# Kernel tuning notes

Measured on AMD Instinct MI355X. Metric: run time of the kernel, lower is better.

Reference implementation:

```python
import jax, jax.numpy as jnp
import numpy as np

COMMITMENT_COST = 0.25


def setup_inputs() -> dict:
    key = jax.random.key(0)
    k1, k2 = jax.random.split(key)
    N, K, D = 131072, 1024, 64
    inputs = jax.random.normal(k1, (N, D), dtype=jnp.float32)
    # torch init: uniform(-1/K, 1/K); use randn scaled similarly-small for a generic table
    embedding = jax.random.uniform(k2, (K, D), dtype=jnp.float32,
                                   minval=-1.0 / K, maxval=1.0 / K)
    return {"inputs": inputs, "embedding": embedding}


def reference(inputs, embedding):
    distances = (jnp.sum(inputs ** 2, axis=1, keepdims=True)
                 + jnp.sum(embedding ** 2, axis=1)
                 - 2.0 * inputs @ embedding.T)
    encoding_indices = jnp.argmin(distances, axis=1)            # [N]
    # direct gather (same math as one-hot @ embedding)
    quantized = embedding[encoding_indices]                     # [N, D]

    diff2 = jnp.mean((quantized - inputs) ** 2)
    # e_latent_loss == q_latent_loss numerically in fwd
    loss = diff2 + COMMITMENT_COST * diff2

    # straight-through output (forward value == quantized)
    quantized_st = inputs + jax.lax.stop_gradient(quantized - inputs)

    # avg_probs via histogram instead of materializing [N, K] one-hot
    N, K = inputs.shape[0], embedding.shape[0]
    counts = jnp.zeros((K,), dtype=jnp.float32).at[encoding_indices].add(1.0)
    avg_probs = counts / N
    perplexity = jnp.exp(-jnp.sum(avg_probs * jnp.log(avg_probs + 1e-10)))

    return quantized_st, loss, encoding_indices.reshape(N, 1), perplexity
```

## Files before the change

kernel.cpp:

```cpp
#include <hip/hip_runtime.h>
#include <hip/hip_bf16.h>

#define D 64
#define MARGIN 4e-5f
#define KS 2

typedef __attribute__((ext_vector_type(8))) short bf16x8;
typedef __attribute__((ext_vector_type(4))) float f32x4;
typedef __attribute__((ext_vector_type(4))) unsigned uint4v;


__device__ __forceinline__ float np_pairwise_sumsq64(const float* a) {
    float r[8];
#pragma unroll
    for (int j = 0; j < 8; ++j) r[j] = __fmul_rn(a[j], a[j]);
#pragma unroll
    for (int i = 8; i < 64; i += 8)
#pragma unroll
        for (int j = 0; j < 8; ++j)
            r[j] = __fadd_rn(r[j], __fmul_rn(a[i + j], a[i + j]));
    return __fadd_rn(
        __fadd_rn(__fadd_rn(r[0], r[1]), __fadd_rn(r[2], r[3])),
        __fadd_rn(__fadd_rn(r[4], r[5]), __fadd_rn(r[6], r[7])));
}

#define CVT8(F0, F1, H, L)                                                    \
    do {                                                                      \
        float _f[8] = {F0.x, F0.y, F0.z, F0.w, F1.x, F1.y, F1.z, F1.w};       \
        _Pragma("unroll") for (int _i = 0; _i < 8; ++_i) {                    \
            unsigned _u = __float_as_uint(_f[_i]);                            \
            unsigned _hb = (_u + 0x7fffu + ((_u >> 16) & 1u)) >> 16;          \
            float _hf = __uint_as_float(_hb << 16);                           \
            float _r = _f[_i] - _hf;                                          \
            unsigned _u2 = __float_as_uint(_r);                               \
            unsigned _lb = (_u2 + 0x7fffu + ((_u2 >> 16) & 1u)) >> 16;        \
            H[_i] = (short)_hb;                                               \
            L[_i] = (short)_lb;                                               \
        }                                                                     \
    } while (0)

__global__ __launch_bounds__(256) void vq_prep_all(
    const float* __restrict__ emb, int K,
    float* __restrict__ eenp, float* __restrict__ neh,
    unsigned short* __restrict__ ehs, float* __restrict__ eT) {
    int b = blockIdx.x;
    if (b < 64) {
        int t = b * 256 + threadIdx.x;
        int tile = t >> 8, r = t & 255, s = r >> 6, l = r & 63;
        int sub = l & 15, grp = l >> 4;
        int k = tile * 16 + sub;
        int d0 = ((s & 1) << 5) + (grp << 3);
        const float* e = emb + (size_t)k * D + d0;
        float4 f0 = *(const float4*)e;
        float4 f1 = *(const float4*)(e + 4);
        bf16x8 h, lo;
        CVT8(f0, f1, h, lo);
        *(bf16x8*)(ehs + (size_t)t * 8) = (s >> 1) ? lo : h;
    } else if (b < 68) {
        int k = (b - 64) * 256 + threadIdx.x;
        float s = np_pairwise_sumsq64(emb + (size_t)k * D);
        eenp[k] = s;
        neh[k] = -0.5f * s;
    } else {
        int t = (b - 68) * 256 + threadIdx.x;
        int d = t / K, k = t - d * K;
        eT[t] = emb[(size_t)k * D + d];
    }
}

__global__ __launch_bounds__(256) void vq_screen(
    const float* __restrict__ x, const unsigned short* __restrict__ ehs,
    const float* __restrict__ neh, int N, int K,
    float* __restrict__ m1p, float* __restrict__ m2p, int* __restrict__ bip,
    float* __restrict__ xxp) {
    const int tid = threadIdx.x;
    const int lane = tid & 63;
    const int wid = tid >> 6;
    const int kslice = blockIdx.x & (KS - 1);
    const int rowblk = blockIdx.x >> 1;
    const int row0 = rowblk * 256 + wid * 64;
    const int sub = lane & 15, grp = lane >> 4;
    const int g4 = grp << 2;
    const int k0 = kslice * (K / KS);
    const int NT = (K / KS) >> 4;
    const int t0 = k0 >> 4;

    __shared__ __align__(16) unsigned short lds[2][2048];

    bf16x8 xh[4][2], xl[4][2];
    float xq[4];
#pragma unroll
    for (int rt = 0; rt < 4; ++rt) {
        xq[rt] = 0.f;
        const float* xrow = x + (((size_t)(row0 + (rt << 4) + sub)) << 6) + (grp << 3);
#pragma unroll
        for (int s = 0; s < 2; ++s) {
            float4 f0 = *(const float4*)(xrow + (s << 5));
            float4 f1 = *(const float4*)(xrow + (s << 5) + 4);
            xq[rt] = fmaf(f0.x, f0.x, xq[rt]); xq[rt] = fmaf(f0.y, f0.y, xq[rt]);
            xq[rt] = fmaf(f0.z, f0.z, xq[rt]); xq[rt] = fmaf(f0.w, f0.w, xq[rt]);
            xq[rt] = fmaf(f1.x, f1.x, xq[rt]); xq[rt] = fmaf(f1.y, f1.y, xq[rt]);
            xq[rt] = fmaf(f1.z, f1.z, xq[rt]); xq[rt] = fmaf(f1.w, f1.w, xq[rt]);
            CVT8(f0, f1, xh[rt][s], xl[rt][s]);
        }
    }
#pragma unroll
    for (int rt = 0; rt < 4; ++rt) {
        xq[rt] += __shfl_xor(xq[rt], 16);
        xq[rt] += __shfl_xor(xq[rt], 32);
    }

    float m1[4], m2[4];
    int bi[4];
#pragma unroll
    for (int rt = 0; rt < 4; ++rt) { m1[rt] = -3e38f; m2[rt] = -3e38f; bi[rt] = 0; }

    const unsigned short* sbase = ehs + ((size_t)t0 << 11);
    const int slot = (wid << 9) + (lane << 3);

    uint4v tmp = *(const uint4v*)(sbase + slot);
    *(uint4v*)&lds[0][slot] = tmp;
    __syncthreads();

    for (int t = 0; t < NT; ++t) {
        const int cur = t & 1;
        if (t + 1 < NT)
            tmp = *(const uint4v*)(sbase + ((size_t)(t + 1) << 11) + slot);

        f32x4 cb = *(const f32x4*)(neh + k0 + (t << 4) + g4);
        const bf16x8* L = (const bf16x8*)&lds[cur][0];
        bf16x8 a0 = L[lane];
        bf16x8 a1 = L[64 + lane];
        bf16x8 a2 = L[128 + lane];
        bf16x8 a3 = L[192 + lane];

        f32x4 acc[4];
#pragma unroll
        for (int rt = 0; rt < 4; ++rt)
            acc[rt] = __builtin_amdgcn_mfma_f32_16x16x32_bf16(a0, xh[rt][0], cb, 0, 0, 0);
#pragma unroll
        for (int rt = 0; rt < 4; ++rt)
            acc[rt] = __builtin_amdgcn_mfma_f32_16x16x32_bf16(a2, xh[rt][0], acc[rt], 0, 0, 0);
#pragma unroll
        for (int rt = 0; rt < 4; ++rt)
            acc[rt] = __builtin_amdgcn_mfma_f32_16x16x32_bf16(a0, xl[rt][0], acc[rt], 0, 0, 0);
#pragma unroll
        for (int rt = 0; rt < 4; ++rt)
            acc[rt] = __builtin_amdgcn_mfma_f32_16x16x32_bf16(a1, xh[rt][1], acc[rt], 0, 0, 0);
#pragma unroll
        for (int rt = 0; rt < 4; ++rt)
            acc[rt] = __builtin_amdgcn_mfma_f32_16x16x32_bf16(a3, xh[rt][1], acc[rt], 0, 0, 0);
#pragma unroll
        for (int rt = 0; rt < 4; ++rt)
            acc[rt] = __builtin_amdgcn_mfma_f32_16x16x32_bf16(a1, xl[rt][1], acc[rt], 0, 0, 0);

        int cbase = k0 + (t << 4) + g4;
#pragma unroll
        for (int rt = 0; rt < 4; ++rt) {
#pragma unroll
            for (int j = 0; j < 4; ++j) {
                float v = acc[rt][j];
                int c = cbase + j;
                bool tk = v > m1[rt];
                m2[rt] = fminf(fmaxf(v, m2[rt]), m1[rt]);
                m1[rt] = tk ? v : m1[rt];
                bi[rt] = tk ? c : bi[rt];
            }
        }

        if (t + 1 < NT)
            *(uint4v*)&lds[cur ^ 1][slot] = tmp;
        __syncthreads();
    }

#pragma unroll
    for (int rt = 0; rt < 4; ++rt) {
#pragma unroll
        for (int off = 16; off <= 32; off <<= 1) {
            float om1 = __shfl_xor(m1[rt], off);
            float om2 = __shfl_xor(m2[rt], off);
            int obi = __shfl_xor(bi[rt], off);
            bool take = (om1 > m1[rt]) || (om1 == m1[rt] && obi < bi[rt]);
            m2[rt] = fmaxf(fminf(om1, m1[rt]), fmaxf(om2, m2[rt]));
            m1[rt] = take ? om1 : m1[rt];
            bi[rt] = take ? obi : bi[rt];
        }
    }

    if (lane < 16) {
#pragma unroll
        for (int rt = 0; rt < 4; ++rt) {
            size_t idx = (size_t)kslice * N + row0 + (rt << 4) + lane;
            m1p[idx] = m1[rt];
            m2p[idx] = m2[rt];
            bip[idx] = bi[rt];
            if (kslice == 0) xxp[row0 + (rt << 4) + lane] = xq[rt];
        }
    }
}

__global__ __launch_bounds__(256) void vq_epilogue(
    const float* __restrict__ x, const float* __restrict__ emb,
    const float* __restrict__ eT, const float* __restrict__ eenp,
    const float* __restrict__ m1p, const float* __restrict__ m2p,
    const int* __restrict__ bip, const float* __restrict__ xxp, int N, int K,
    float* __restrict__ outq, float* __restrict__ outidx,
    double* __restrict__ loss) {
    const int tid = threadIdx.x;
    const int rows0 = blockIdx.x * 64;
    __shared__ int sdec[64];
    __shared__ int samb[64];
    __shared__ int snamb;
    __shared__ float sxrow[64];
    __shared__ float swm[4];
    __shared__ int swi[4];

    if (tid == 0) snamb = 0;

    if (tid < 64) {
        int r = rows0 + tid;
        float gm1 = m1p[r], gm2 = m2p[r];
        int gbi = bip[r];
        {
            size_t idx = (size_t)N + r;
            float m1b = m1p[idx], m2b = m2p[idx];
            int bb = bip[idx];
            bool take = m1b > gm1;
            gm2 = fmaxf(fminf(gm1, m1b), fmaxf(gm2, m2b));
            gm1 = take ? m1b : gm1;
            gbi = take ? bb : gbi;
        }
        int dec = gbi;
        double lpart = 0.0;
        if (2.0f * (gm1 - gm2) < MARGIN) {
            int pos = atomicAdd(&snamb, 1);
            samb[pos] = tid;
            dec = -1;
        } else {
            outidx[r] = (float)dec;
            lpart = (double)(xxp[r] - 2.0f * gm1);
        }
        sdec[tid] = dec;
#pragma unroll
        for (int off = 32; off; off >>= 1) lpart += __shfl_down(lpart, off);
        if (tid == 0) atomicAdd(loss, lpart);
    }
    __syncthreads();

    const int namb = snamb;
    const int w = tid >> 6, l = tid & 63;
    const int c4 = (w << 6) + l;
    const f32x4* eT4 = (const f32x4*)eT;
    for (int j = 0; j < namb; ++j) {
        int lr = samb[j];
        int row = rows0 + lr;
        if (tid < 64) sxrow[tid] = x[(size_t)row * D + tid];
        __syncthreads();
        float xx = np_pairwise_sumsq64(sxrow);
        f32x4 dt = (f32x4){0.f, 0.f, 0.f, 0.f};
#pragma unroll 8
        for (int d = 0; d < D; ++d) {
            f32x4 ev = eT4[(size_t)d * 256 + c4];
            float xv = sxrow[d];
            dt[0] = __fmaf_rn(xv, ev[0], dt[0]);
            dt[1] = __fmaf_rn(xv, ev[1], dt[1]);
            dt[2] = __fmaf_rn(xv, ev[2], dt[2]);
            dt[3] = __fmaf_rn(xv, ev[3], dt[3]);
        }
        float bm = 1e30f;
        int bi = 0;
#pragma unroll
        for (int jj = 0; jj < 4; ++jj) {
            int k = (c4 << 2) + jj;
            float dist = __fsub_rn(__fadd_rn(xx, eenp[k]),
                                   __fmul_rn(2.0f, dt[jj]));
            if (dist < bm) { bm = dist; bi = k; }
        }
#pragma unroll
        for (int off = 1; off < 64; off <<= 1) {
            float ov = __shfl_xor(bm, off);
            int oi = __shfl_xor(bi, off);
            if (ov < bm || (ov == bm && oi < bi)) { bm = ov; bi = oi; }
        }
        if (l == 0) { swm[w] = bm; swi[w] = bi; }
        __syncthreads();
        if (tid == 0) {
            float fm = swm[0];
            int fi = swi[0];
#pragma unroll
            for (int ww = 1; ww < 4; ++ww) {
                float ov = swm[ww];
                int oi = swi[ww];
                if (ov < fm || (ov == fm && oi < fi)) { fm = ov; fi = oi; }
            }
            sdec[lr] = fi;
            outidx[row] = (float)fi;
            atomicAdd(loss, (double)fm);
        }
        __syncthreads();
    }

    const int chunk = tid & 15, rl = tid >> 4;
#pragma unroll
    for (int p = 0; p < 4; ++p) {
        int lr = p * 16 + rl;
        int dp = sdec[lr];
        if (dp >= 0) {
            float4 ev = *(const float4*)(emb + (size_t)dp * D + chunk * 4);
            *(float4*)(outq + (size_t)(rows0 + lr) * D + chunk * 4) = ev;
        }
    }
}

__global__ __launch_bounds__(256) void vq_histperp(
    const float* __restrict__ outidx, int N, int K,
    unsigned* __restrict__ counts, unsigned* __restrict__ done,
    const double* __restrict__ loss,
    float* __restrict__ out_loss, float* __restrict__ out_perp) {
    __shared__ unsigned h[1024];
    __shared__ unsigned rank_s;
#pragma unroll
    for (int i = 0; i < 4; ++i) h[threadIdx.x + 256 * i] = 0;
    __syncthreads();
    int per = N / gridDim.x;
    int base = blockIdx.x * per;
    for (int i = threadIdx.x; i < per; i += 256) {
        int k = (int)outidx[base + i];
        atomicAdd(&h[k], 1u);
    }
    __syncthreads();
#pragma unroll
    for (int i = 0; i < 4; ++i) {
        int b = threadIdx.x + 256 * i;
        unsigned v = h[b];
        if (b < K && v) atomicAdd(counts + b, v);
    }
    __threadfence();
    if (threadIdx.x == 0) rank_s = atomicAdd(done, 1u);
    __syncthreads();
    if (rank_s == gridDim.x - 1) {
        double part = 0.0;
        for (int k = threadIdx.x; k < K; k += 256) {
            unsigned c = atomicAdd(counts + k, 0u);
            double p = (double)c / (double)N;
            part += p * log(p + 1e-10);
        }
#pragma unroll
        for (int off = 32; off; off >>= 1) part += __shfl_down(part, off);
        __shared__ double ls[4];
        if ((threadIdx.x & 63) == 0) ls[threadIdx.x >> 6] = part;
        __syncthreads();
        if (threadIdx.x == 0) {
            double s = ls[0] + ls[1] + ls[2] + ls[3];
            *out_perp = (float)exp(-s);
            double diff2 = *loss / ((double)N * (double)D);
            *out_loss = (float)(1.25 * diff2);
        }
    }
}

extern "C" void kernel_launch(void* const* d_in, const int* in_sizes, int n_in,
                              void* d_out, int out_size, void* d_ws, size_t ws_size,
                              hipStream_t stream) {
    const float* x = (const float*)d_in[0];
    const float* emb = (const float*)d_in[1];
    int N = in_sizes[0] / D;
    int K = in_sizes[1] / D;

    float* outq = (float*)d_out;
    float* out_loss = outq + (size_t)N * D;
    float* outidx = out_loss + 1;
    float* out_perp = outidx + N;

    char* ws = (char*)d_ws;
    unsigned* counts = (unsigned*)ws;
    unsigned* done = (unsigned*)(ws + (size_t)K * 4);
    double* loss = (double*)(ws + (size_t)K * 4 + 8);
    float* neh = (float*)(ws + (size_t)K * 4 + 16);
    float* eenp = (float*)(ws + (size_t)K * 8 + 16);
    unsigned short* ehs = (unsigned short*)(ws + (size_t)K * 12 + 16);
    float* eT = (float*)(ws + (size_t)K * 12 + 16 + (size_t)K * 256);
    size_t poff = (size_t)K * 12 + 16 + (size_t)K * 256 + (size_t)K * D * 4;
    float* m1p = (float*)(ws + poff);
    float* m2p = (float*)(ws + poff + (size_t)KS * N * 4);
    int* bip = (int*)(ws + poff + (size_t)KS * N * 8);
    float* xxp = (float*)(ws + poff + (size_t)KS * N * 12);

    hipMemsetAsync(d_ws, 0, (size_t)K * 4 + 16, stream);

    vq_prep_all<<<64 + 4 + (K * D + 255) / 256, 256, 0, stream>>>(
        emb, K, eenp, neh, ehs, eT);
    vq_screen<<<(N / 256) * KS, 256, 0, stream>>>(x, ehs, neh, N, K,
                                                  m1p, m2p, bip, xxp);
    vq_epilogue<<<N / 64, 256, 0, stream>>>(x, emb, eT, eenp, m1p, m2p, bip,
                                            xxp, N, K, outq, outidx, loss);
    vq_histperp<<<16, 256, 0, stream>>>(outidx, N, K, counts, done, loss,
                                        out_loss, out_perp);
}
```

Measured before the change: 177.9 us.

## Move ambiguous-row fp32 rescoring into separate compacted-worklist kernel

```diff
diff --git a/kernel.cpp b/kernel.cpp
--- a/kernel.cpp
+++ b/kernel.cpp
@@ -200,22 +200,15 @@
 }
 
 __global__ __launch_bounds__(256) void vq_epilogue(
-    const float* __restrict__ x, const float* __restrict__ emb,
-    const float* __restrict__ eT, const float* __restrict__ eenp,
+    const float* __restrict__ emb,
     const float* __restrict__ m1p, const float* __restrict__ m2p,
-    const int* __restrict__ bip, const float* __restrict__ xxp, int N, int K,
+    const int* __restrict__ bip, const float* __restrict__ xxp, int N,
     float* __restrict__ outq, float* __restrict__ outidx,
-    double* __restrict__ loss) {
+    double* __restrict__ lossA,
+    unsigned* __restrict__ nunc, unsigned* __restrict__ list) {
     const int tid = threadIdx.x;
     const int rows0 = blockIdx.x * 64;
     __shared__ int sdec[64];
-    __shared__ int samb[64];
-    __shared__ int snamb;
-    __shared__ float sxrow[64];
-    __shared__ float swm[4];
-    __shared__ int swi[4];
-
-    if (tid == 0) snamb = 0;
 
     if (tid < 64) {
         int r = rows0 + tid;
@@ -230,11 +223,17 @@
             gm1 = take ? m1b : gm1;
             gbi = take ? bb : gbi;
         }
+        bool amb = 2.0f * (gm1 - gm2) < MARGIN;
+        unsigned long long mask = __ballot(amb);
+        int cnt = __popcll(mask);
+        unsigned base = 0;
+        if (tid == 0 && cnt) base = atomicAdd(nunc, (unsigned)cnt);
+        base = __shfl(base, 0);
         int dec = gbi;
         double lpart = 0.0;
-        if (2.0f * (gm1 - gm2) < MARGIN) {
-            int pos = atomicAdd(&snamb, 1);
-            samb[pos] = tid;
+        if (amb) {
+            int rank = __popcll(mask & ((1ull << tid) - 1ull));
+            list[base + rank] = (unsigned)r;
             dec = -1;
         } else {
             outidx[r] = (float)dec;
@@ -243,62 +242,9 @@
         sdec[tid] = dec;
 #pragma unroll
         for (int off = 32; off; off >>= 1) lpart += __shfl_down(lpart, off);
-        if (tid == 0) atomicAdd(loss, lpart);
-    }
-    __syncthreads();
-
-    const int namb = snamb;
-    const int w = tid >> 6, l = tid & 63;
-    const int c4 = (w << 6) + l;
-    const f32x4* eT4 = (const f32x4*)eT;
-    for (int j = 0; j < namb; ++j) {
-        int lr = samb[j];
-        int row = rows0 + lr;
-        if (tid < 64) sxrow[tid] = x[(size_t)row * D + tid];
-        __syncthreads();
-        float xx = np_pairwise_sumsq64(sxrow);
-        f32x4 dt = (f32x4){0.f, 0.f, 0.f, 0.f};
-#pragma unroll 8
-        for (int d = 0; d < D; ++d) {
-            f32x4 ev = eT4[(size_t)d * 256 + c4];
-            float xv = sxrow[d];
-            dt[0] = __fmaf_rn(xv, ev[0], dt[0]);
-            dt[1] = __fmaf_rn(xv, ev[1], dt[1]);
-            dt[2] = __fmaf_rn(xv, ev[2], dt[2]);
-            dt[3] = __fmaf_rn(xv, ev[3], dt[3]);
-        }
-        float bm = 1e30f;
-        int bi = 0;
-#pragma unroll
-        for (int jj = 0; jj < 4; ++jj) {
-            int k = (c4 << 2) + jj;
-            float dist = __fsub_rn(__fadd_rn(xx, eenp[k]),
-                                   __fmul_rn(2.0f, dt[jj]));
-            if (dist < bm) { bm = dist; bi = k; }
-        }
-#pragma unroll
-        for (int off = 1; off < 64; off <<= 1) {
-            float ov = __shfl_xor(bm, off);
-            int oi = __shfl_xor(bi, off);
-            if (ov < bm || (ov == bm && oi < bi)) { bm = ov; bi = oi; }
-        }
-        if (l == 0) { swm[w] = bm; swi[w] = bi; }
-        __syncthreads();
-        if (tid == 0) {
-            float fm = swm[0];
-            int fi = swi[0];
-#pragma unroll
-            for (int ww = 1; ww < 4; ++ww) {
-                float ov = swm[ww];
-                int oi = swi[ww];
-                if (ov < fm || (ov == fm && oi < fi)) { fm = ov; fi = oi; }
-            }
-            sdec[lr] = fi;
-            outidx[row] = (float)fi;
-            atomicAdd(loss, (double)fm);
-        }
-        __syncthreads();
-    }
+        if (tid == 0) lossA[blockIdx.x] = lpart;
+    }
+    __syncthreads();
 
     const int chunk = tid & 15, rl = tid >> 4;
 #pragma unroll
@@ -312,10 +258,81 @@
     }
 }
 
+__global__ __launch_bounds__(256) void vq_resolve(
+    const float* __restrict__ x, const float* __restrict__ emb,
+    const float* __restrict__ eT, const float* __restrict__ eenp,
+    int N, int K,
+    float* __restrict__ outq, float* __restrict__ outidx,
+    double* __restrict__ lossR,
+    const unsigned* __restrict__ nunc, const unsigned* __restrict__ list) {
+    const unsigned n = *nunc;
+    const int w = threadIdx.x >> 6, lane = threadIdx.x & 63;
+    const f32x4* eT4 = (const f32x4*)eT;
+    double lp = 0.0;
+    for (unsigned i = blockIdx.x * 4 + w; i < n; i += gridDim.x * 4) {
+        const int r = (int)list[i];
+        float xr[D];
+        {
+            const float4* xp = (const float4*)(x + (size_t)r * D);
+#pragma unroll
+            for (int jj = 0; jj < D / 4; ++jj) {
+                float4 v = xp[jj];
+                xr[4 * jj + 0] = v.x; xr[4 * jj + 1] = v.y;
+                xr[4 * jj + 2] = v.z; xr[4 * jj + 3] = v.w;
+            }
+        }
+        float xx = np_pairwise_sumsq64(xr);
+        f32x4 dt[4];
+#pragma unroll
+        for (int kk = 0; kk < 4; ++kk) dt[kk] = (f32x4){0.f, 0.f, 0.f, 0.f};
+#pragma unroll 4
+        for (int d = 0; d < D; ++d) {
+            float xv = xr[d];
+#pragma unroll
+            for (int kk = 0; kk < 4; ++kk) {
+                f32x4 ev = eT4[(size_t)d * 256 + kk * 64 + lane];
+                dt[kk][0] = __fmaf_rn(xv, ev[0], dt[kk][0]);
+                dt[kk][1] = __fmaf_rn(xv, ev[1], dt[kk][1]);
+                dt[kk][2] = __fmaf_rn(xv, ev[2], dt[kk][2]);
+                dt[kk][3] = __fmaf_rn(xv, ev[3], dt[kk][3]);
+            }
+        }
+        float bm = 1e30f;
+        int bi = 0;
+#pragma unroll
+        for (int kk = 0; kk < 4; ++kk)
+#pragma unroll
+            for (int jj = 0; jj < 4; ++jj) {
+                int k = kk * 256 + lane * 4 + jj;
+                float dist = __fsub_rn(__fadd_rn(xx, eenp[k]),
+                                       __fmul_rn(2.0f, dt[kk][jj]));
+                if (dist < bm) { bm = dist; bi = k; }
+            }
+#pragma unroll
+        for (int off = 1; off < 64; off <<= 1) {
+            float ov = __shfl_xor(bm, off);
+            int oi = __shfl_xor(bi, off);
+            if (ov < bm || (ov == bm && oi < bi)) { bm = ov; bi = oi; }
+        }
+        float ev = emb[(size_t)bi * D + lane];
+        outq[(size_t)r * D + lane] = ev;
+        if (lane == 0) {
+            outidx[r] = (float)bi;
+            lp += (double)bm;
+        }
+    }
+    __shared__ double lsw[4];
+    if (lane == 0) lsw[w] = lp;
+    __syncthreads();
+    if (threadIdx.x == 0)
+        lossR[blockIdx.x] = lsw[0] + lsw[1] + lsw[2] + lsw[3];
+}
+
 __global__ __launch_bounds__(256) void vq_histperp(
     const float* __restrict__ outidx, int N, int K,
     unsigned* __restrict__ counts, unsigned* __restrict__ done,
-    const double* __restrict__ loss,
+    const double* __restrict__ lossA, int nA,
+    const double* __restrict__ lossR, int nR,
     float* __restrict__ out_loss, float* __restrict__ out_perp) {
     __shared__ unsigned h[1024];
     __shared__ unsigned rank_s;
@@ -345,16 +362,25 @@
             double p = (double)c / (double)N;
             part += p * log(p + 1e-10);
         }
-#pragma unroll
-        for (int off = 32; off; off >>= 1) part += __shfl_down(part, off);
-        __shared__ double ls[4];
-        if ((threadIdx.x & 63) == 0) ls[threadIdx.x >> 6] = part;
+        double lsum = 0.0;
+        for (int i = threadIdx.x; i < nA; i += 256) lsum += lossA[i];
+        for (int i = threadIdx.x; i < nR; i += 256) lsum += lossR[i];
+#pragma unroll
+        for (int off = 32; off; off >>= 1) {
+            part += __shfl_down(part, off);
+            lsum += __shfl_down(lsum, off);
+        }
+        __shared__ double ls[4], ls2[4];
+        if ((threadIdx.x & 63) == 0) {
+            ls[threadIdx.x >> 6] = part;
+            ls2[threadIdx.x >> 6] = lsum;
+        }
         __syncthreads();
         if (threadIdx.x == 0) {
             double s = ls[0] + ls[1] + ls[2] + ls[3];
+            double L = ls2[0] + ls2[1] + ls2[2] + ls2[3];
             *out_perp = (float)exp(-s);
-            double diff2 = *loss / ((double)N * (double)D);
-            *out_loss = (float)(1.25 * diff2);
+            *out_loss = (float)(1.25 * (L / ((double)N * (double)D)));
         }
     }
 }
@@ -375,16 +401,20 @@
     char* ws = (char*)d_ws;
     unsigned* counts = (unsigned*)ws;
     unsigned* done = (unsigned*)(ws + (size_t)K * 4);
-    double* loss = (double*)(ws + (size_t)K * 4 + 8);
-    float* neh = (float*)(ws + (size_t)K * 4 + 16);
-    float* eenp = (float*)(ws + (size_t)K * 8 + 16);
-    unsigned short* ehs = (unsigned short*)(ws + (size_t)K * 12 + 16);
-    float* eT = (float*)(ws + (size_t)K * 12 + 16 + (size_t)K * 256);
-    size_t poff = (size_t)K * 12 + 16 + (size_t)K * 256 + (size_t)K * D * 4;
-    float* m1p = (float*)(ws + poff);
-    float* m2p = (float*)(ws + poff + (size_t)KS * N * 4);
-    int* bip = (int*)(ws + poff + (size_t)KS * N * 8);
-    float* xxp = (float*)(ws + poff + (size_t)KS * N * 12);
+    unsigned* nunc = (unsigned*)(ws + (size_t)K * 4 + 4);
+    size_t off = (size_t)K * 4 + 16;
+    float* neh = (float*)(ws + off);            off += (size_t)K * 4;
+    float* eenp = (float*)(ws + off);           off += (size_t)K * 4;
+    unsigned short* ehs = (unsigned short*)(ws + off);  off += (size_t)K * 256;
+    float* eT = (float*)(ws + off);              off += (size_t)K * D * 4;
+    float* m1p = (float*)(ws + off);             off += (size_t)KS * N * 4;
+    float* m2p = (float*)(ws + off);             off += (size_t)KS * N * 4;
+    int* bip = (int*)(ws + off);                 off += (size_t)KS * N * 4;
+    float* xxp = (float*)(ws + off);             off += (size_t)N * 4;
+    unsigned* list = (unsigned*)(ws + off);      off += (size_t)N * 4;
+    int nA = N / 64, nR = 1024;
+    double* lossA = (double*)(ws + off);         off += (size_t)nA * 8;
+    double* lossR = (double*)(ws + off);         off += (size_t)nR * 8;
 
     hipMemsetAsync(d_ws, 0, (size_t)K * 4 + 16, stream);
 
@@ -392,8 +422,11 @@
         emb, K, eenp, neh, ehs, eT);
     vq_screen<<<(N / 256) * KS, 256, 0, stream>>>(x, ehs, neh, N, K,
                                                   m1p, m2p, bip, xxp);
-    vq_epilogue<<<N / 64, 256, 0, stream>>>(x, emb, eT, eenp, m1p, m2p, bip,
-                                            xxp, N, K, outq, outidx, loss);
-    vq_histperp<<<16, 256, 0, stream>>>(outidx, N, K, counts, done, loss,
+    vq_epilogue<<<N / 64, 256, 0, stream>>>(emb, m1p, m2p, bip, xxp, N,
+                                            outq, outidx, lossA, nunc, list);
+    vq_resolve<<<1024, 256, 0, stream>>>(x, emb, eT, eenp, N, K,
+                                         outq, outidx, lossR, nunc, list);
+    vq_histperp<<<16, 256, 0, stream>>>(outidx, N, K, counts, done,
+                                        lossA, nA, lossR, nR,
                                         out_loss, out_perp);
 }
```

New measurement: 190.0 us. +6.8%, slower.
